# Optimization experiments

Measured on AMD Instinct MI355X. Metric: run time of the kernel, lower is better.

The kernel has to match this reference:

```python
import jax, jax.numpy as jnp
import numpy as np
import math

HIDDEN = 768
LABEL_NUM = 16
N_HEADS = 12
HEAD_DIM = HIDDEN // N_HEADS


def setup_inputs() -> dict:
    key = jax.random.key(0)
    ks = jax.random.split(key, 8)
    B, S, L, Ls, H = 8, 128, LABEL_NUM, 8, HIDDEN
    std = 1.0 / math.sqrt(H)
    return {
        "token_embs": jax.random.normal(ks[0], (B, S, H), jnp.float32),
        "label_embs": jax.random.normal(ks[1], (L, Ls, H), jnp.float32),
        "token_mask": jnp.ones((B, S), jnp.float32),
        "label_mask": jnp.ones((L, Ls), jnp.float32),
        "Wq": jax.random.normal(ks[2], (H, H), jnp.float32) * std,
        "bq": jnp.zeros((H,), jnp.float32),
        "Wk": jax.random.normal(ks[3], (H, H), jnp.float32) * std,
        "bk": jnp.zeros((H,), jnp.float32),
        "Wv": jax.random.normal(ks[4], (H, H), jnp.float32) * std,
        "bv": jnp.zeros((H,), jnp.float32),
    }


def reference(token_embs, label_embs, token_mask, label_mask, Wq, bq, Wk, bk, Wv, bv):
    B, S, H = token_embs.shape
    L, Ls, _ = label_embs.shape
    T = S + Ls
    # broadcast (instead of repeat) then concat: [B, L, T, H] -> [B*L, T, H]
    tok = jnp.broadcast_to(token_embs[:, None, :, :], (B, L, S, H))
    lab = jnp.broadcast_to(label_embs[None, :, :, :], (B, L, Ls, H))
    x = jnp.concatenate([tok, lab], axis=2).reshape(B * L, T, H)
    # mask: [B*L, T]; extended additive mask (1-m)*-10000
    tm = jnp.broadcast_to(token_mask[:, None, :], (B, L, S))
    lm = jnp.broadcast_to(label_mask[None, :, :], (B, L, Ls))
    mask = jnp.concatenate([tm, lm], axis=2).reshape(B * L, T)
    bias = (1.0 - mask) * -10000.0  # [BL, T]
    # QKV (torch Linear: y = x W^T + b)
    q = (x @ Wq.T + bq).reshape(B * L, T, N_HEADS, HEAD_DIM)
    k = (x @ Wk.T + bk).reshape(B * L, T, N_HEADS, HEAD_DIM)
    v = (x @ Wv.T + bv).reshape(B * L, T, N_HEADS, HEAD_DIM)
    scores = jnp.einsum("bthd,bshd->bhts", q, k) / math.sqrt(HEAD_DIM)
    scores = scores + bias[:, None, None, :]
    probs = jax.nn.softmax(scores, axis=-1)
    ctx = jnp.einsum("bhts,bshd->bthd", probs, v).reshape(B * L, T, H)
    # [B, L, T, H] -> [B, T, L, H]
    fused = ctx.reshape(B, L, T, H).transpose(0, 2, 1, 3)
    return (fused,)
```

## Files before the change

### kernel.cpp

```cpp
#include <hip/hip_runtime.h>
#include <hip/hip_bf16.h>
#include <stdint.h>

#define HIDDEN 768
#define NH 12
#define HD 64
#define BB 8
#define SS 128
#define LL 16
#define LS 8
#define TT 136
#define NROWS 1152
#define BH (BB * NH)

typedef __attribute__((ext_vector_type(8))) short bf16x8;
typedef __attribute__((ext_vector_type(4))) float f32x4;
typedef __attribute__((ext_vector_type(16))) float f32x16;
typedef __hip_bfloat16 bf16;

__device__ inline float tof(bf16 x) { return __bfloat162float(x); }
__device__ inline uint16_t b16bits(float f) {
    bf16 h = __float2bfloat16(f);
    union { bf16 h; uint16_t u; } u; u.h = h; return u.u;
}

#define TOK_V4 196608
#define XB_V4  221184
#define W_V4   147456
__global__ __launch_bounds__(256) void cast_kernel(
    const float* __restrict__ tok, const float* __restrict__ lab,
    const float* __restrict__ Wq, const float* __restrict__ Wk,
    const float* __restrict__ Wv,
    uint16_t* __restrict__ Xb, uint16_t* __restrict__ Wb)
{
    int g = blockIdx.x * 256 + threadIdx.x;
    float4 v;
    ushort4* d;
    if (g < XB_V4) {
        v = (g < TOK_V4) ? reinterpret_cast<const float4*>(tok)[g]
                         : reinterpret_cast<const float4*>(lab)[g - TOK_V4];
        d = reinterpret_cast<ushort4*>(Xb) + g;
    } else {
        int w = g - XB_V4;
        v = (w < W_V4)     ? reinterpret_cast<const float4*>(Wq)[w]
          : (w < 2 * W_V4) ? reinterpret_cast<const float4*>(Wk)[w - W_V4]
                           : reinterpret_cast<const float4*>(Wv)[w - 2 * W_V4];
        d = reinterpret_cast<ushort4*>(Wb) + w;
    }
    ushort4 h;
    h.x = b16bits(v.x); h.y = b16bits(v.y); h.z = b16bits(v.z); h.w = b16bits(v.w);
    *d = h;
}

__global__ __launch_bounds__(256) void qkv_kernel(
    const uint16_t* __restrict__ Xb, const uint16_t* __restrict__ Wb,
    const float* __restrict__ bq, const float* __restrict__ bk,
    const float* __restrict__ bv,
    bf16* __restrict__ Qw, bf16* __restrict__ Kw, bf16* __restrict__ Vw)
{
    __shared__ __align__(16) uint16_t As[2][64 * 72];
    __shared__ __align__(16) uint16_t Bs[2][128 * 72];

    int tid = threadIdx.x;
    int lane = tid & 63, wv = tid >> 6;
    int ml = lane & 15, quad = lane >> 4;
    int mt = blockIdx.x / 18, nt = blockIdx.x % 18;
    int wr = wv >> 1, wc = wv & 1;

    int mat = nt / 6;
    int col0 = (nt % 6) * 128;
    const float* bptr = (mat == 0) ? bq : ((mat == 1) ? bk : bv);
    bf16* obase       = (mat == 0) ? Qw : ((mat == 1) ? Kw : Vw);

    const uint16_t* asrc = Xb + (size_t)mt * 64 * HIDDEN;
    const uint16_t* bsrc = Wb + (size_t)nt * 128 * HIDDEN;

    int ar_[2], ac_[2], br_[4], bc_[4];
    #pragma unroll
    for (int i = 0; i < 2; ++i) { int g = i * 256 + tid; ar_[i] = g >> 3; ac_[i] = (g & 7) * 8; }
    #pragma unroll
    for (int i = 0; i < 4; ++i) { int g = i * 256 + tid; br_[i] = g >> 3; bc_[i] = (g & 7) * 8; }

    bf16x8 ra[2], rb[4];
    #pragma unroll
    for (int i = 0; i < 2; ++i)
        ra[i] = *reinterpret_cast<const bf16x8*>(asrc + (size_t)ar_[i] * HIDDEN + ac_[i]);
    #pragma unroll
    for (int i = 0; i < 4; ++i)
        rb[i] = *reinterpret_cast<const bf16x8*>(bsrc + (size_t)br_[i] * HIDDEN + bc_[i]);

    f32x4 acc[2][4] = {};
    int p = 0;

    for (int k0 = 0; k0 < HIDDEN; k0 += 64) {
        #pragma unroll
        for (int i = 0; i < 2; ++i)
            *reinterpret_cast<bf16x8*>(&As[p][ar_[i] * 72 + ac_[i]]) = ra[i];
        #pragma unroll
        for (int i = 0; i < 4; ++i)
            *reinterpret_cast<bf16x8*>(&Bs[p][br_[i] * 72 + bc_[i]]) = rb[i];
        __syncthreads();

        if (k0 + 64 < HIDDEN) {
            #pragma unroll
            for (int i = 0; i < 2; ++i)
                ra[i] = *reinterpret_cast<const bf16x8*>(asrc + (size_t)ar_[i] * HIDDEN + k0 + 64 + ac_[i]);
            #pragma unroll
            for (int i = 0; i < 4; ++i)
                rb[i] = *reinterpret_cast<const bf16x8*>(bsrc + (size_t)br_[i] * HIDDEN + k0 + 64 + bc_[i]);
        }

        #pragma unroll
        for (int kh = 0; kh < 2; ++kh) {
            bf16x8 af[2], bfr[4];
            #pragma unroll
            for (int rt = 0; rt < 2; ++rt)
                af[rt] = *reinterpret_cast<const bf16x8*>(&As[p][(wr * 32 + rt * 16 + ml) * 72 + kh * 32 + quad * 8]);
            #pragma unroll
            for (int ct = 0; ct < 4; ++ct)
                bfr[ct] = *reinterpret_cast<const bf16x8*>(&Bs[p][(wc * 64 + ct * 16 + ml) * 72 + kh * 32 + quad * 8]);
            #pragma unroll
            for (int rt = 0; rt < 2; ++rt)
                #pragma unroll
                for (int ct = 0; ct < 4; ++ct)
                    acc[rt][ct] = __builtin_amdgcn_mfma_f32_16x16x32_bf16(af[rt], bfr[ct], acc[rt][ct], 0, 0, 0);
        }
        p ^= 1;
    }

    #pragma unroll
    for (int ct = 0; ct < 4; ++ct) {
        int c = col0 + wc * 64 + ct * 16 + ml;
        float bvv = bptr[c];
        #pragma unroll
        for (int rt = 0; rt < 2; ++rt) {
            #pragma unroll
            for (int reg = 0; reg < 4; ++reg) {
                int R = mt * 64 + wr * 32 + rt * 16 + quad * 4 + reg;
                obase[(size_t)R * HIDDEN + c] = __float2bfloat16(acc[rt][ct][reg] + bvv);
            }
        }
    }
}

__global__ __launch_bounds__(256) void attn_tt_kernel(
    const bf16* __restrict__ Qw, const bf16* __restrict__ Kw,
    const bf16* __restrict__ Vw, const float* __restrict__ tmask,
    bf16* __restrict__ ctx_tt, float* __restrict__ m_tt, float* __restrict__ d_tt,
    uint32_t* __restrict__ Vt_g)
{
    __shared__ __align__(16) uint32_t KldsW[128 * 36];
    __shared__ __align__(16) uint32_t VtW[64 * 68];
    __shared__ __align__(16) uint32_t PW[4][16 * 68];
    __shared__ float bias_s[128];

    int bh = blockIdx.x >> 1;
    int hf = blockIdx.x & 1;
    int b = bh / NH, h = bh % NH;
    int tid = threadIdx.x;
    int lane = tid & 63, wv = tid >> 6;
    int ml = lane & 15, quad = lane >> 4;

    for (int i = tid; i < 128 * 32; i += 256) {
        int s = i >> 5, w = i & 31;
        KldsW[s * 36 + w] =
            reinterpret_cast<const uint32_t*>(Kw + (size_t)(b * SS + s) * HIDDEN + h * HD)[w];
    }
    #pragma unroll
    for (int c = 0; c < 8; ++c) {
        int g = c * 256 + tid;
        int s2 = g >> 5, dw = g & 31;
        const uint32_t* v0 = reinterpret_cast<const uint32_t*>(Vw + (size_t)(b * SS + 2 * s2) * HIDDEN + h * HD);
        const uint32_t* v1 = reinterpret_cast<const uint32_t*>(Vw + (size_t)(b * SS + 2 * s2 + 1) * HIDDEN + h * HD);
        uint32_t a = v0[dw], bb = v1[dw];
        VtW[(2 * dw) * 68 + s2]     = (a & 0xffffu) | ((bb & 0xffffu) << 16);
        VtW[(2 * dw + 1) * 68 + s2] = (a >> 16) | (bb & 0xffff0000u);
    }
    for (int i = tid; i < 128; i += 256)
        bias_s[i] = (1.0f - tmask[b * SS + i]) * -10000.0f;
    __syncthreads();

    if (hf == 0) {
        uint32_t* vg = Vt_g + (size_t)bh * 4096;
        #pragma unroll
        for (int c = 0; c < 16; ++c) {
            int g = c * 256 + tid;
            vg[g] = VtW[(g >> 6) * 68 + (g & 63)];
        }
    }

    const bf16* Klb = reinterpret_cast<const bf16*>(KldsW);
    const bf16* Vtb = reinterpret_cast<const bf16*>(VtW);
    const bf16* Pb  = reinterpret_cast<const bf16*>(PW[wv]);

    int qr = hf * 64 + wv * 16 + ml;
    const bf16* qp = Qw + (size_t)(b * SS + qr) * HIDDEN + h * HD + quad * 8;
    bf16x8 a0 = *reinterpret_cast<const bf16x8*>(qp);
    bf16x8 a1 = *reinterpret_cast<const bf16x8*>(qp + 32);

    f32x4 sc[8];
    #pragma unroll
    for (int ct = 0; ct < 8; ++ct) {
        const bf16* kp = Klb + (ct * 16 + ml) * 72 + quad * 8;
        bf16x8 b0 = *reinterpret_cast<const bf16x8*>(kp);
        bf16x8 b1 = *reinterpret_cast<const bf16x8*>(kp + 32);
        f32x4 z = {0.f, 0.f, 0.f, 0.f};
        z = __builtin_amdgcn_mfma_f32_16x16x32_bf16(a0, b0, z, 0, 0, 0);
        z = __builtin_amdgcn_mfma_f32_16x16x32_bf16(a1, b1, z, 0, 0, 0);
        sc[ct] = z;
    }

    float mx[4] = {-1e30f, -1e30f, -1e30f, -1e30f};
    #pragma unroll
    for (int ct = 0; ct < 8; ++ct) {
        float bc = bias_s[ct * 16 + ml];
        #pragma unroll
        for (int reg = 0; reg < 4; ++reg) {
            float v = sc[ct][reg] * 0.125f + bc;
            sc[ct][reg] = v;
            mx[reg] = fmaxf(mx[reg], v);
        }
    }
    #pragma unroll
    for (int reg = 0; reg < 4; ++reg)
        #pragma unroll
        for (int off = 1; off < 16; off <<= 1)
            mx[reg] = fmaxf(mx[reg], __shfl_xor(mx[reg], off));

    float Zs[4] = {0.f, 0.f, 0.f, 0.f};
    #pragma unroll
    for (int ct = 0; ct < 8; ++ct) {
        #pragma unroll
        for (int reg = 0; reg < 4; ++reg) {
            float e = __expf(sc[ct][reg] - mx[reg]);
            sc[ct][reg] = e;
            Zs[reg] += e;
        }
    }
    #pragma unroll
    for (int reg = 0; reg < 4; ++reg)
        #pragma unroll
        for (int off = 1; off < 16; off <<= 1)
            Zs[reg] += __shfl_xor(Zs[reg], off);

    #pragma unroll
    for (int reg = 0; reg < 4; ++reg) {
        int gr = bh * 128 + hf * 64 + wv * 16 + quad * 4 + reg;
        if (ml == 0) { m_tt[gr] = mx[reg]; d_tt[gr] = Zs[reg]; }
    }

    #pragma unroll
    for (int ct = 0; ct < 8; ++ct) {
        #pragma unroll
        for (int reg = 0; reg < 4; ++reg) {
            float e = sc[ct][reg];
            float ep = __shfl_xor(e, 1);
            if ((ml & 1) == 0)
                PW[wv][(quad * 4 + reg) * 68 + ct * 8 + (ml >> 1)] =
                    (uint32_t)b16bits(e) | ((uint32_t)b16bits(ep) << 16);
        }
    }

    float rZ[4];
    #pragma unroll
    for (int reg = 0; reg < 4; ++reg) rZ[reg] = 1.0f / Zs[reg];

    #pragma unroll
    for (int ct4 = 0; ct4 < 4; ++ct4) {
        f32x4 acc = {0.f, 0.f, 0.f, 0.f};
        #pragma unroll
        for (int ks = 0; ks < 4; ++ks) {
            bf16x8 ap = *reinterpret_cast<const bf16x8*>(Pb + ml * 136 + ks * 32 + quad * 8);
            bf16x8 bp = *reinterpret_cast<const bf16x8*>(Vtb + (ct4 * 16 + ml) * 136 + ks * 32 + quad * 8);
            acc = __builtin_amdgcn_mfma_f32_16x16x32_bf16(ap, bp, acc, 0, 0, 0);
        }
        #pragma unroll
        for (int reg = 0; reg < 4; ++reg) {
            int gr = bh * 128 + hf * 64 + wv * 16 + quad * 4 + reg;
            ctx_tt[(size_t)gr * 64 + ct4 * 16 + ml] = __float2bfloat16(acc[reg] * rZ[reg]);
        }
    }
}

__global__ __launch_bounds__(256) void attn_merge_kernel(
    const bf16* __restrict__ Qw, const bf16* __restrict__ Kw,
    const bf16* __restrict__ Vw, const uint32_t* __restrict__ Vt_g,
    const bf16* __restrict__ ctx_tt, const float* __restrict__ m_tt,
    const float* __restrict__ d_tt,
    const float* __restrict__ tmask, const float* __restrict__ lmask,
    float* __restrict__ out)
{
    __shared__ __align__(16) uint32_t VtW[64 * 84];
    __shared__ __align__(16) uint32_t PWL[16 * 84];
    __shared__ __align__(16) uint32_t P2W[4][32 * 8];
    __shared__ float wtab[4][32], itab[4][32];
    __shared__ float mtt_s[128], dtt_s[128], bias_t[128];
    __shared__ float bias_l[16];

    int p = blockIdx.x & 7;
    int h = (blockIdx.x >> 3) % NH;
    int b = blockIdx.x / (8 * NH);
    int l0 = 2 * p, l1 = l0 + 1;
    int bh = b * NH + h;
    int tid = threadIdx.x;
    int lane = tid & 63, wv = tid >> 6;
    int ml = lane & 15, quad = lane >> 4;
    int hl = lane & 31, hi = lane >> 5;

    {
        const uint32_t* vg = Vt_g + (size_t)bh * 4096;
        #pragma unroll
        for (int c = 0; c < 16; ++c) {
            int g = c * 256 + tid;
            VtW[(g >> 6) * 84 + (g & 63)] = vg[g];
        }
    }
    for (int g = tid; g < 512; g += 256) {
        int d = g >> 3, jj = g & 7;
        int s0 = 128 + 2 * jj, s1 = s0 + 1;
        int r0 = (s0 < 136) ? (1024 + l0 * LS + (s0 - 128)) : (1024 + l1 * LS + (s0 - 136));
        int r1 = (s1 < 136) ? (1024 + l0 * LS + (s1 - 128)) : (1024 + l1 * LS + (s1 - 136));
        uint16_t lo = reinterpret_cast<const uint16_t*>(Vw + (size_t)r0 * HIDDEN + h * HD)[d];
        uint16_t hi2 = reinterpret_cast<const uint16_t*>(Vw + (size_t)r1 * HIDDEN + h * HD)[d];
        VtW[d * 84 + 64 + jj] = (uint32_t)lo | ((uint32_t)hi2 << 16);
    }
    for (int g = tid; g < 512; g += 256)
        VtW[(g >> 3) * 84 + 72 + (g & 7)] = 0;

    if (tid < 128) {
        mtt_s[tid] = m_tt[bh * 128 + tid];
        dtt_s[tid] = d_tt[bh * 128 + tid];
        bias_t[tid] = (1.0f - tmask[b * SS + tid]) * -10000.0f;
    }
    if (tid < 16) {
        int labk = (tid < 8) ? (l0 * LS + tid) : (l1 * LS + tid - 8);
        bias_l[tid] = (1.0f - lmask[labk]) * -10000.0f;
    }
    if (tid < 128)
        PWL[(tid >> 3) * 84 + 72 + (tid & 7)] = 0;
    __syncthreads();

    const bf16* Vtb = reinterpret_cast<const bf16*>(VtW);

    int kprow = 1024 + ((ml < 8) ? (l0 * LS + ml) : (l1 * LS + ml - 8));
    const bf16* kpp = Kw + (size_t)kprow * HIDDEN + h * HD + quad * 8;
    bf16x8 kb0 = *reinterpret_cast<const bf16x8*>(kpp);
    bf16x8 kb1 = *reinterpret_cast<const bf16x8*>(kpp + 32);

    if (wv < 3) {
        const bf16* P2b = reinterpret_cast<const bf16*>(P2W[wv]);
        for (int rt = wv; rt < 8; rt += 3) {
            int tq = rt * 16 + ml;
            const bf16* qp = Qw + (size_t)(b * SS + tq) * HIDDEN + h * HD + quad * 8;
            bf16x8 a0 = *reinterpret_cast<const bf16x8*>(qp);
            bf16x8 a1 = *reinterpret_cast<const bf16x8*>(qp + 32);

            f32x4 z = {0.f, 0.f, 0.f, 0.f};
            z = __builtin_amdgcn_mfma_f32_16x16x32_bf16(a0, kb0, z, 0, 0, 0);
            z = __builtin_amdgcn_mfma_f32_16x16x32_bf16(a1, kb1, z, 0, 0, 0);

            #pragma unroll
            for (int reg = 0; reg < 4; ++reg) {
                int trow = quad * 4 + reg;
                float s = z[reg] * 0.125f + bias_l[ml];
                float m = s;
                m = fmaxf(m, __shfl_xor(m, 1));
                m = fmaxf(m, __shfl_xor(m, 2));
                m = fmaxf(m, __shfl_xor(m, 4));
                float mtt = mtt_s[rt * 16 + trow], dtt = dtt_s[rt * 16 + trow];
                float m_new = fmaxf(mtt, m);
                float e = __expf(s - m_new);
                float dh = e;
                dh += __shfl_xor(dh, 1);
                dh += __shfl_xor(dh, 2);
                dh += __shfl_xor(dh, 4);
                float alpha = __expf(mtt - m_new);
                float w = alpha * dtt;
                float inv = 1.0f / (w + dh);
                if (ml == 0) { wtab[wv][trow] = w;      itab[wv][trow] = inv; }
                if (ml == 8) { wtab[wv][16 + trow] = w; itab[wv][16 + trow] = inv; }
                float ep = __shfl_xor(e, 1);
                if ((ml & 1) == 0) {
                    uint32_t pk = (uint32_t)b16bits(e) | ((uint32_t)b16bits(ep) << 16);
                    P2W[wv][trow * 8 + (ml >> 1)]        = (ml < 8) ? pk : 0u;
                    P2W[wv][(16 + trow) * 8 + (ml >> 1)] = (ml < 8) ? 0u : pk;
                }
            }

            bf16x8 ap  = *reinterpret_cast<const bf16x8*>(P2b + hl * 16 + hi * 8);
            bf16x8 bv0 = *reinterpret_cast<const bf16x8*>(Vtb + hl * 168 + 128 + hi * 8);
            bf16x8 bv1 = *reinterpret_cast<const bf16x8*>(Vtb + (32 + hl) * 168 + 128 + hi * 8);
            f32x16 c0 = {}, c1 = {};
            c0 = __builtin_amdgcn_mfma_f32_32x32x16_bf16(ap, bv0, c0, 0, 0, 0);
            c1 = __builtin_amdgcn_mfma_f32_32x32x16_bf16(ap, bv1, c1, 0, 0, 0);

            float cv0[8], cv1[8];
            #pragma unroll
            for (int reg = 0; reg < 8; ++reg) {
                int row = (reg & 3) + 8 * (reg >> 2) + 4 * hi;
                const bf16* cp = ctx_tt + (size_t)(bh * 128 + rt * 16 + row) * 64;
                cv0[reg] = tof(cp[hl]);
                cv1[reg] = tof(cp[32 + hl]);
            }
            #pragma unroll
            for (int reg = 0; reg < 16; ++reg) {
                int row = (reg & 3) + 8 * (reg >> 2) + 4 * hi;
                int trow = row & 15;
                int lsel = (row < 16) ? l0 : l1;
                float w = wtab[wv][row], inv = itab[wv][row];
                float c0v = (reg < 8) ? cv0[reg] : cv0[reg - 8];
                float c1v = (reg < 8) ? cv1[reg] : cv1[reg - 8];
                size_t ob = (((size_t)b * TT + rt * 16 + trow) * LL + lsel) * HIDDEN + h * HD;
                out[ob + hl]      = (w * c0v + c0[reg]) * inv;
                out[ob + 32 + hl] = (w * c1v + c1[reg]) * inv;
            }
        }
    } else {
        const bf16* Pb = reinterpret_cast<const bf16*>(PWL);
        int qrow = 1024 + ((ml < 8) ? (l0 * LS + ml) : (l1 * LS + ml - 8));
        const bf16* qp = Qw + (size_t)qrow * HIDDEN + h * HD + quad * 8;
        bf16x8 a0 = *reinterpret_cast<const bf16x8*>(qp);
        bf16x8 a1 = *reinterpret_cast<const bf16x8*>(qp + 32);

        f32x4 sc[9];
        #pragma unroll
        for (int ct = 0; ct < 9; ++ct) {
            bf16x8 b0, b1;
            if (ct < 8) {
                const bf16* kp = Kw + (size_t)(b * SS + ct * 16 + ml) * HIDDEN + h * HD + quad * 8;
                b0 = *reinterpret_cast<const bf16x8*>(kp);
                b1 = *reinterpret_cast<const bf16x8*>(kp + 32);
            } else { b0 = kb0; b1 = kb1; }
            f32x4 zz = {0.f, 0.f, 0.f, 0.f};
            zz = __builtin_amdgcn_mfma_f32_16x16x32_bf16(a0, b0, zz, 0, 0, 0);
            zz = __builtin_amdgcn_mfma_f32_16x16x32_bf16(a1, b1, zz, 0, 0, 0);
            sc[ct] = zz;
        }

        float mx[4] = {-1e30f, -1e30f, -1e30f, -1e30f};
        #pragma unroll
        for (int ct = 0; ct < 9; ++ct) {
            #pragma unroll
            for (int reg = 0; reg < 4; ++reg) {
                int rq = quad * 4 + reg;
                float bc = (ct < 8) ? bias_t[ct * 16 + ml]
                                    : (((rq < 8) != (ml < 8)) ? -1e30f : bias_l[ml]);
                float v = sc[ct][reg] * 0.125f + bc;
                sc[ct][reg] = v;
                mx[reg] = fmaxf(mx[reg], v);
            }
        }
        #pragma unroll
        for (int reg = 0; reg < 4; ++reg)
            #pragma unroll
            for (int off = 1; off < 16; off <<= 1)
                mx[reg] = fmaxf(mx[reg], __shfl_xor(mx[reg], off));

        float Zs[4] = {0.f, 0.f, 0.f, 0.f};
        #pragma unroll
        for (int ct = 0; ct < 9; ++ct) {
            #pragma unroll
            for (int reg = 0; reg < 4; ++reg) {
                float e = __expf(sc[ct][reg] - mx[reg]);
                sc[ct][reg] = e;
                Zs[reg] += e;
            }
        }
        #pragma unroll
        for (int reg = 0; reg < 4; ++reg)
            #pragma unroll
            for (int off = 1; off < 16; off <<= 1)
                Zs[reg] += __shfl_xor(Zs[reg], off);
        float zi[4];
        #pragma unroll
        for (int reg = 0; reg < 4; ++reg) zi[reg] = 1.0f / Zs[reg];

        #pragma unroll
        for (int ct = 0; ct < 9; ++ct) {
            #pragma unroll
            for (int reg = 0; reg < 4; ++reg) {
                float e = sc[ct][reg];
                float ep = __shfl_xor(e, 1);
                if ((ml & 1) == 0)
                    PWL[(quad * 4 + reg) * 84 + ct * 8 + (ml >> 1)] =
                        (uint32_t)b16bits(e) | ((uint32_t)b16bits(ep) << 16);
            }
        }

        #pragma unroll
        for (int ct4 = 0; ct4 < 4; ++ct4) {
            f32x4 acc = {0.f, 0.f, 0.f, 0.f};
            #pragma unroll
            for (int ks = 0; ks < 5; ++ks) {
                bf16x8 ap = *reinterpret_cast<const bf16x8*>(Pb + ml * 168 + ks * 32 + quad * 8);
                bf16x8 bp = *reinterpret_cast<const bf16x8*>(Vtb + (ct4 * 16 + ml) * 168 + ks * 32 + quad * 8);
                acc = __builtin_amdgcn_mfma_f32_16x16x32_bf16(ap, bp, acc, 0, 0, 0);
            }
            #pragma unroll
            for (int reg = 0; reg < 4; ++reg) {
                int rq = quad * 4 + reg;
                int l = (rq < 8) ? l0 : l1;
                int t = SS + (rq & 7);
                out[(((size_t)b * TT + t) * LL + l) * HIDDEN + h * HD + ct4 * 16 + ml] =
                    acc[reg] * zi[reg];
            }
        }
    }
}

extern "C" void kernel_launch(void* const* d_in, const int* in_sizes, int n_in,
                              void* d_out, int out_size, void* d_ws, size_t ws_size,
                              hipStream_t stream)
{
    const float* tok   = (const float*)d_in[0];
    const float* lab   = (const float*)d_in[1];
    const float* tmask = (const float*)d_in[2];
    const float* lmask = (const float*)d_in[3];
    const float* Wq    = (const float*)d_in[4];
    const float* bq    = (const float*)d_in[5];
    const float* Wk    = (const float*)d_in[6];
    const float* bk    = (const float*)d_in[7];
    const float* Wv    = (const float*)d_in[8];
    const float* bv    = (const float*)d_in[9];

    bf16* Qw = (bf16*)d_ws;
    bf16* Kw = Qw + (size_t)NROWS * HIDDEN;
    bf16* Vw = Kw + (size_t)NROWS * HIDDEN;
    bf16* ctx = Vw + (size_t)NROWS * HIDDEN;
    float* m_tt = (float*)(ctx + (size_t)BH * 128 * 64);
    float* d_tt = m_tt + BH * 128;
    uint32_t* Vt_g = (uint32_t*)(d_tt + BH * 128);
    uint16_t* Xb = (uint16_t*)(Vt_g + (size_t)BH * 4096);
    uint16_t* Wb = Xb + (size_t)NROWS * HIDDEN;

    cast_kernel<<<dim3(2592), 256, 0, stream>>>(tok, lab, Wq, Wk, Wv, Xb, Wb);
    qkv_kernel<<<dim3(18 * 18), 256, 0, stream>>>(
        Xb, Wb, bq, bk, bv, Qw, Kw, Vw);
    attn_tt_kernel<<<dim3(BH * 2), 256, 0, stream>>>(
        Qw, Kw, Vw, tmask, ctx, m_tt, d_tt, Vt_g);
    attn_merge_kernel<<<dim3(BB * NH * 8), 256, 0, stream>>>(
        Qw, Kw, Vw, Vt_g, ctx, m_tt, d_tt, tmask, lmask, (float*)d_out);
}
```

Measured before the change: 129.5 us.

## Process two label pairs per merge block to reuse staged V and ctx loads

```diff
diff --git a/kernel.cpp b/kernel.cpp
--- a/kernel.cpp
+++ b/kernel.cpp
@@ -292,18 +292,15 @@
 {
     __shared__ __align__(16) uint32_t VtW[64 * 84];
     __shared__ __align__(16) uint32_t PWL[16 * 84];
-    __shared__ __align__(16) uint32_t P2W[4][32 * 8];
-    __shared__ float wtab[4][32], itab[4][32];
+    __shared__ __align__(16) uint32_t P2W[3][32 * 8];
+    __shared__ float wtab[3][32], itab[3][32];
     __shared__ float mtt_s[128], dtt_s[128], bias_t[128];
-    __shared__ float bias_l[16];
-
-    int p = blockIdx.x & 7;
-    int h = (blockIdx.x >> 3) % NH;
-    int b = blockIdx.x / (8 * NH);
-    int l0 = 2 * p, l1 = l0 + 1;
-    int bh = b * NH + h;
+    __shared__ float bias_l[2][16];
+
+    int bh = blockIdx.x % 96, pp = blockIdx.x / 96;
+    int b = bh / NH, h = bh % NH;
     int tid = threadIdx.x;
-    int lane = tid & 63, wv = tid >> 6;
+    int lane = tid & 63, wvi = tid >> 6;
     int ml = lane & 15, quad = lane >> 4;
     int hl = lane & 31, hi = lane >> 5;
 
@@ -315,84 +312,51 @@
             VtW[(g >> 6) * 84 + (g & 63)] = vg[g];
         }
     }
-    for (int g = tid; g < 512; g += 256) {
-        int d = g >> 3, jj = g & 7;
+    for (int g = tid; g < 1024; g += 256) {
+        int d = g >> 4, slot = g & 15;
+        int it = slot >> 3, jj = slot & 7;
+        int lp = pp + it * 4;
+        int l0 = 2 * lp, l1 = l0 + 1;
         int s0 = 128 + 2 * jj, s1 = s0 + 1;
         int r0 = (s0 < 136) ? (1024 + l0 * LS + (s0 - 128)) : (1024 + l1 * LS + (s0 - 136));
         int r1 = (s1 < 136) ? (1024 + l0 * LS + (s1 - 128)) : (1024 + l1 * LS + (s1 - 136));
-        uint16_t lo = reinterpret_cast<const uint16_t*>(Vw + (size_t)r0 * HIDDEN + h * HD)[d];
+        uint16_t lo  = reinterpret_cast<const uint16_t*>(Vw + (size_t)r0 * HIDDEN + h * HD)[d];
         uint16_t hi2 = reinterpret_cast<const uint16_t*>(Vw + (size_t)r1 * HIDDEN + h * HD)[d];
-        VtW[d * 84 + 64 + jj] = (uint32_t)lo | ((uint32_t)hi2 << 16);
-    }
-    for (int g = tid; g < 512; g += 256)
-        VtW[(g >> 3) * 84 + 72 + (g & 7)] = 0;
-
+        VtW[d * 84 + 64 + it * 8 + jj] = (uint32_t)lo | ((uint32_t)hi2 << 16);
+    }
     if (tid < 128) {
         mtt_s[tid] = m_tt[bh * 128 + tid];
         dtt_s[tid] = d_tt[bh * 128 + tid];
         bias_t[tid] = (1.0f - tmask[b * SS + tid]) * -10000.0f;
     }
-    if (tid < 16) {
-        int labk = (tid < 8) ? (l0 * LS + tid) : (l1 * LS + tid - 8);
-        bias_l[tid] = (1.0f - lmask[labk]) * -10000.0f;
-    }
-    if (tid < 128)
-        PWL[(tid >> 3) * 84 + 72 + (tid & 7)] = 0;
+    if (tid < 32) {
+        int it = tid >> 4, j = tid & 15;
+        int lp = pp + it * 4;
+        int labk = (j < 8) ? (2 * lp * LS + j) : ((2 * lp + 1) * LS + j - 8);
+        bias_l[it][j] = (1.0f - lmask[labk]) * -10000.0f;
+    }
     __syncthreads();
 
     const bf16* Vtb = reinterpret_cast<const bf16*>(VtW);
 
-    int kprow = 1024 + ((ml < 8) ? (l0 * LS + ml) : (l1 * LS + ml - 8));
-    const bf16* kpp = Kw + (size_t)kprow * HIDDEN + h * HD + quad * 8;
-    bf16x8 kb0 = *reinterpret_cast<const bf16x8*>(kpp);
-    bf16x8 kb1 = *reinterpret_cast<const bf16x8*>(kpp + 32);
-
-    if (wv < 3) {
-        const bf16* P2b = reinterpret_cast<const bf16*>(P2W[wv]);
-        for (int rt = wv; rt < 8; rt += 3) {
+    bf16x8 kbA[2], kbB[2];
+    #pragma unroll
+    for (int it = 0; it < 2; ++it) {
+        int lp = pp + it * 4;
+        int l0 = 2 * lp, l1 = l0 + 1;
+        int kprow = 1024 + ((ml < 8) ? (l0 * LS + ml) : (l1 * LS + ml - 8));
+        const bf16* kpp = Kw + (size_t)kprow * HIDDEN + h * HD + quad * 8;
+        kbA[it] = *reinterpret_cast<const bf16x8*>(kpp);
+        kbB[it] = *reinterpret_cast<const bf16x8*>(kpp + 32);
+    }
+
+    if (wvi < 3) {
+        const bf16* P2b = reinterpret_cast<const bf16*>(P2W[wvi]);
+        for (int rt = wvi; rt < 8; rt += 3) {
             int tq = rt * 16 + ml;
             const bf16* qp = Qw + (size_t)(b * SS + tq) * HIDDEN + h * HD + quad * 8;
             bf16x8 a0 = *reinterpret_cast<const bf16x8*>(qp);
             bf16x8 a1 = *reinterpret_cast<const bf16x8*>(qp + 32);
-
-            f32x4 z = {0.f, 0.f, 0.f, 0.f};
-            z = __builtin_amdgcn_mfma_f32_16x16x32_bf16(a0, kb0, z, 0, 0, 0);
-            z = __builtin_amdgcn_mfma_f32_16x16x32_bf16(a1, kb1, z, 0, 0, 0);
-
-            #pragma unroll
-            for (int reg = 0; reg < 4; ++reg) {
-                int trow = quad * 4 + reg;
-                float s = z[reg] * 0.125f + bias_l[ml];
-                float m = s;
-                m = fmaxf(m, __shfl_xor(m, 1));
-                m = fmaxf(m, __shfl_xor(m, 2));
-                m = fmaxf(m, __shfl_xor(m, 4));
-                float mtt = mtt_s[rt * 16 + trow], dtt = dtt_s[rt * 16 + trow];
-                float m_new = fmaxf(mtt, m);
-                float e = __expf(s - m_new);
-                float dh = e;
-                dh += __shfl_xor(dh, 1);
-                dh += __shfl_xor(dh, 2);
-                dh += __shfl_xor(dh, 4);
-                float alpha = __expf(mtt - m_new);
-                float w = alpha * dtt;
-                float inv = 1.0f / (w + dh);
-                if (ml == 0) { wtab[wv][trow] = w;      itab[wv][trow] = inv; }
-                if (ml == 8) { wtab[wv][16 + trow] = w; itab[wv][16 + trow] = inv; }
-                float ep = __shfl_xor(e, 1);
-                if ((ml & 1) == 0) {
-                    uint32_t pk = (uint32_t)b16bits(e) | ((uint32_t)b16bits(ep) << 16);
-                    P2W[wv][trow * 8 + (ml >> 1)]        = (ml < 8) ? pk : 0u;
-                    P2W[wv][(16 + trow) * 8 + (ml >> 1)] = (ml < 8) ? 0u : pk;
-                }
-            }
-
-            bf16x8 ap  = *reinterpret_cast<const bf16x8*>(P2b + hl * 16 + hi * 8);
-            bf16x8 bv0 = *reinterpret_cast<const bf16x8*>(Vtb + hl * 168 + 128 + hi * 8);
-            bf16x8 bv1 = *reinterpret_cast<const bf16x8*>(Vtb + (32 + hl) * 168 + 128 + hi * 8);
-            f32x16 c0 = {}, c1 = {};
-            c0 = __builtin_amdgcn_mfma_f32_32x32x16_bf16(ap, bv0, c0, 0, 0, 0);
-            c1 = __builtin_amdgcn_mfma_f32_32x32x16_bf16(ap, bv1, c1, 0, 0, 0);
 
             float cv0[8], cv1[8];
             #pragma unroll
@@ -402,107 +366,165 @@
                 cv0[reg] = tof(cp[hl]);
                 cv1[reg] = tof(cp[32 + hl]);
             }
-            #pragma unroll
-            for (int reg = 0; reg < 16; ++reg) {
-                int row = (reg & 3) + 8 * (reg >> 2) + 4 * hi;
-                int trow = row & 15;
-                int lsel = (row < 16) ? l0 : l1;
-                float w = wtab[wv][row], inv = itab[wv][row];
-                float c0v = (reg < 8) ? cv0[reg] : cv0[reg - 8];
-                float c1v = (reg < 8) ? cv1[reg] : cv1[reg - 8];
-                size_t ob = (((size_t)b * TT + rt * 16 + trow) * LL + lsel) * HIDDEN + h * HD;
-                out[ob + hl]      = (w * c0v + c0[reg]) * inv;
-                out[ob + 32 + hl] = (w * c1v + c1[reg]) * inv;
+
+            #pragma unroll
+            for (int it = 0; it < 2; ++it) {
+                int lp = pp + it * 4;
+                int l0 = 2 * lp, l1 = l0 + 1;
+
+                f32x4 z = {0.f, 0.f, 0.f, 0.f};
+                z = __builtin_amdgcn_mfma_f32_16x16x32_bf16(a0, kbA[it], z, 0, 0, 0);
+                z = __builtin_amdgcn_mfma_f32_16x16x32_bf16(a1, kbB[it], z, 0, 0, 0);
+
+                #pragma unroll
+                for (int reg = 0; reg < 4; ++reg) {
+                    int trow = quad * 4 + reg;
+                    float s = z[reg] * 0.125f + bias_l[it][ml];
+                    float m = s;
+                    m = fmaxf(m, __shfl_xor(m, 1));
+                    m = fmaxf(m, __shfl_xor(m, 2));
+                    m = fmaxf(m, __shfl_xor(m, 4));
+                    float mtt = mtt_s[rt * 16 + trow], dtt = dtt_s[rt * 16 + trow];
+                    float m_new = fmaxf(mtt, m);
+                    float e = __expf(s - m_new);
+                    float dh = e;
+                    dh += __shfl_xor(dh, 1);
+                    dh += __shfl_xor(dh, 2);
+                    dh += __shfl_xor(dh, 4);
+                    float alpha = __expf(mtt - m_new);
+                    float w = alpha * dtt;
+                    float inv = 1.0f / (w + dh);
+                    if (ml == 0) { wtab[wvi][trow] = w;      itab[wvi][trow] = inv; }
+                    if (ml == 8) { wtab[wvi][16 + trow] = w; itab[wvi][16 + trow] = inv; }
+                    float ep = __shfl_xor(e, 1);
+                    if ((ml & 1) == 0) {
+                        uint32_t pk = (uint32_t)b16bits(e) | ((uint32_t)b16bits(ep) << 16);
+                        P2W[wvi][trow * 8 + (ml >> 1)]        = (ml < 8) ? pk : 0u;
+                        P2W[wvi][(16 + trow) * 8 + (ml >> 1)] = (ml < 8) ? 0u : pk;
+                    }
+                }
+
+                bf16x8 ap  = *reinterpret_cast<const bf16x8*>(P2b + hl * 16 + hi * 8);
+                bf16x8 bv0 = *reinterpret_cast<const bf16x8*>(Vtb + hl * 168 + 128 + it * 16 + hi * 8);
+                bf16x8 bv1 = *reinterpret_cast<const bf16x8*>(Vtb + (32 + hl) * 168 + 128 + it * 16 + hi * 8);
+                f32x16 c0 = {}, c1 = {};
+                c0 = __builtin_amdgcn_mfma_f32_32x32x16_bf16(ap, bv0, c0, 0, 0, 0);
+                c1 = __builtin_amdgcn_mfma_f32_32x32x16_bf16(ap, bv1, c1, 0, 0, 0);
+
+                #pragma unroll
+                for (int reg = 0; reg < 16; ++reg) {
+                    int row = (reg & 3) + 8 * (reg >> 2) + 4 * hi;
+                    int trow = row & 15;
+                    int lsel = (row < 16) ? l0 : l1;
+                    float w = wtab[wvi][row], inv = itab[wvi][row];
+                    float c0v = (reg < 8) ? cv0[reg] : cv0[reg - 8];
+                    float c1v = (reg < 8) ? cv1[reg] : cv1[reg - 8];
+                    size_t ob = (((size_t)b * TT + rt * 16 + trow) * LL + lsel) * HIDDEN + h * HD;
+                    out[ob + hl]      = (w * c0v + c0[reg]) * inv;
+                    out[ob + 32 + hl] = (w * c1v + c1[reg]) * inv;
+                }
             }
         }
     } else {
         const bf16* Pb = reinterpret_cast<const bf16*>(PWL);
-        int qrow = 1024 + ((ml < 8) ? (l0 * LS + ml) : (l1 * LS + ml - 8));
-        const bf16* qp = Qw + (size_t)qrow * HIDDEN + h * HD + quad * 8;
-        bf16x8 a0 = *reinterpret_cast<const bf16x8*>(qp);
-        bf16x8 a1 = *reinterpret_cast<const bf16x8*>(qp + 32);
-
-        f32x4 sc[9];
-        #pragma unroll
-        for (int ct = 0; ct < 9; ++ct) {
-            bf16x8 b0, b1;
-            if (ct < 8) {
-                const bf16* kp = Kw + (size_t)(b * SS + ct * 16 + ml) * HIDDEN + h * HD + quad * 8;
-                b0 = *reinterpret_cast<const bf16x8*>(kp);
-                b1 = *reinterpret_cast<const bf16x8*>(kp + 32);
-            } else { b0 = kb0; b1 = kb1; }
-            f32x4 zz = {0.f, 0.f, 0.f, 0.f};
-            zz = __builtin_amdgcn_mfma_f32_16x16x32_bf16(a0, b0, zz, 0, 0, 0);
-            zz = __builtin_amdgcn_mfma_f32_16x16x32_bf16(a1, b1, zz, 0, 0, 0);
-            sc[ct] = zz;
-        }
-
-        float mx[4] = {-1e30f, -1e30f, -1e30f, -1e30f};
-        #pragma unroll
-        for (int ct = 0; ct < 9; ++ct) {
-            #pragma unroll
-            for (int reg = 0; reg < 4; ++reg) {
-                int rq = quad * 4 + reg;
-                float bc = (ct < 8) ? bias_t[ct * 16 + ml]
-                                    : (((rq < 8) != (ml < 8)) ? -1e30f : bias_l[ml]);
-                float v = sc[ct][reg] * 0.125f + bc;
-                sc[ct][reg] = v;
-                mx[reg] = fmaxf(mx[reg], v);
-            }
-        }
-        #pragma unroll
-        for (int reg = 0; reg < 4; ++reg)
-            #pragma unroll
-            for (int off = 1; off < 16; off <<= 1)
-                mx[reg] = fmaxf(mx[reg], __shfl_xor(mx[reg], off));
-
-        float Zs[4] = {0.f, 0.f, 0.f, 0.f};
-        #pragma unroll
-        for (int ct = 0; ct < 9; ++ct) {
-            #pragma unroll
-            for (int reg = 0; reg < 4; ++reg) {
-                float e = __expf(sc[ct][reg] - mx[reg]);
-                sc[ct][reg] = e;
-                Zs[reg] += e;
-            }
-        }
-        #pragma unroll
-        for (int reg = 0; reg < 4; ++reg)
-            #pragma unroll
-            for (int off = 1; off < 16; off <<= 1)
-                Zs[reg] += __shfl_xor(Zs[reg], off);
-        float zi[4];
-        #pragma unroll
-        for (int reg = 0; reg < 4; ++reg) zi[reg] = 1.0f / Zs[reg];
-
-        #pragma unroll
-        for (int ct = 0; ct < 9; ++ct) {
-            #pragma unroll
-            for (int reg = 0; reg < 4; ++reg) {
-                float e = sc[ct][reg];
-                float ep = __shfl_xor(e, 1);
-                if ((ml & 1) == 0)
-                    PWL[(quad * 4 + reg) * 84 + ct * 8 + (ml >> 1)] =
-                        (uint32_t)b16bits(e) | ((uint32_t)b16bits(ep) << 16);
-            }
-        }
-
-        #pragma unroll
-        for (int ct4 = 0; ct4 < 4; ++ct4) {
-            f32x4 acc = {0.f, 0.f, 0.f, 0.f};
-            #pragma unroll
-            for (int ks = 0; ks < 5; ++ks) {
-                bf16x8 ap = *reinterpret_cast<const bf16x8*>(Pb + ml * 168 + ks * 32 + quad * 8);
-                bf16x8 bp = *reinterpret_cast<const bf16x8*>(Vtb + (ct4 * 16 + ml) * 168 + ks * 32 + quad * 8);
-                acc = __builtin_amdgcn_mfma_f32_16x16x32_bf16(ap, bp, acc, 0, 0, 0);
-            }
-            #pragma unroll
-            for (int reg = 0; reg < 4; ++reg) {
-                int rq = quad * 4 + reg;
-                int l = (rq < 8) ? l0 : l1;
-                int t = SS + (rq & 7);
-                out[(((size_t)b * TT + t) * LL + l) * HIDDEN + h * HD + ct4 * 16 + ml] =
-                    acc[reg] * zi[reg];
+        #pragma unroll
+        for (int it = 0; it < 2; ++it) {
+            int lp = pp + it * 4;
+            int l0 = 2 * lp, l1 = l0 + 1;
+
+            for (int z2 = lane; z2 < 128; z2 += 64) {
+                int row = z2 >> 3, col = z2 & 7;
+                PWL[row * 84 + 64 + (1 - it) * 8 + col] = 0;
+            }
+
+            int qrow = 1024 + ((ml < 8) ? (l0 * LS + ml) : (l1 * LS + ml - 8));
+            const bf16* qp = Qw + (size_t)qrow * HIDDEN + h * HD + quad * 8;
+            bf16x8 a0 = *reinterpret_cast<const bf16x8*>(qp);
+            bf16x8 a1 = *reinterpret_cast<const bf16x8*>(qp + 32);
+
+            f32x4 sc[9];
+            #pragma unroll
+            for (int ct = 0; ct < 9; ++ct) {
+                bf16x8 b0, b1;
+                if (ct < 8) {
+                    const bf16* kp = Kw + (size_t)(b * SS + ct * 16 + ml) * HIDDEN + h * HD + quad * 8;
+                    b0 = *reinterpret_cast<const bf16x8*>(kp);
+                    b1 = *reinterpret_cast<const bf16x8*>(kp + 32);
+                } else { b0 = kbA[it]; b1 = kbB[it]; }
+                f32x4 zz = {0.f, 0.f, 0.f, 0.f};
+                zz = __builtin_amdgcn_mfma_f32_16x16x32_bf16(a0, b0, zz, 0, 0, 0);
+                zz = __builtin_amdgcn_mfma_f32_16x16x32_bf16(a1, b1, zz, 0, 0, 0);
+                sc[ct] = zz;
+            }
+
+            float mx[4] = {-1e30f, -1e30f, -1e30f, -1e30f};
+            #pragma unroll
+            for (int ct = 0; ct < 9; ++ct) {
+                #pragma unroll
+                for (int reg = 0; reg < 4; ++reg) {
+                    int rq = quad * 4 + reg;
+                    float bc = (ct < 8) ? bias_t[ct * 16 + ml]
+                                        : (((rq < 8) != (ml < 8)) ? -1e30f : bias_l[it][ml]);
+                    float v = sc[ct][reg] * 0.125f + bc;
+                    sc[ct][reg] = v;
+                    mx[reg] = fmaxf(mx[reg], v);
+                }
+            }
+            #pragma unroll
+            for (int reg = 0; reg < 4; ++reg)
+                #pragma unroll
+                for (int off = 1; off < 16; off <<= 1)
+                    mx[reg] = fmaxf(mx[reg], __shfl_xor(mx[reg], off));
+
+            float Zs[4] = {0.f, 0.f, 0.f, 0.f};
+            #pragma unroll
+            for (int ct = 0; ct < 9; ++ct) {
+                #pragma unroll
+                for (int reg = 0; reg < 4; ++reg) {
+                    float e = __expf(sc[ct][reg] - mx[reg]);
+                    sc[ct][reg] = e;
+                    Zs[reg] += e;
+                }
+            }
+            #pragma unroll
+            for (int reg = 0; reg < 4; ++reg)
+                #pragma unroll
+                for (int off = 1; off < 16; off <<= 1)
+                    Zs[reg] += __shfl_xor(Zs[reg], off);
+            float zi[4];
+            #pragma unroll
+            for (int reg = 0; reg < 4; ++reg) zi[reg] = 1.0f / Zs[reg];
+
+            #pragma unroll
+            for (int ct = 0; ct < 9; ++ct) {
+                int cbase = (ct < 8) ? ct * 8 : (64 + it * 8);
+                #pragma unroll
+                for (int reg = 0; reg < 4; ++reg) {
+                    float e = sc[ct][reg];
+                    float ep = __shfl_xor(e, 1);
+                    if ((ml & 1) == 0)
+                        PWL[(quad * 4 + reg) * 84 + cbase + (ml >> 1)] =
+                            (uint32_t)b16bits(e) | ((uint32_t)b16bits(ep) << 16);
+                }
+            }
+
+            #pragma unroll
+            for (int ct4 = 0; ct4 < 4; ++ct4) {
+                f32x4 acc = {0.f, 0.f, 0.f, 0.f};
+                #pragma unroll
+                for (int ks = 0; ks < 5; ++ks) {
+                    bf16x8 ap = *reinterpret_cast<const bf16x8*>(Pb + ml * 168 + ks * 32 + quad * 8);
+                    bf16x8 bp = *reinterpret_cast<const bf16x8*>(Vtb + (ct4 * 16 + ml) * 168 + ks * 32 + quad * 8);
+                    acc = __builtin_amdgcn_mfma_f32_16x16x32_bf16(ap, bp, acc, 0, 0, 0);
+                }
+                #pragma unroll
+                for (int reg = 0; reg < 4; ++reg) {
+                    int rq = quad * 4 + reg;
+                    int l = (rq < 8) ? l0 : l1;
+                    int t = SS + (rq & 7);
+                    out[(((size_t)b * TT + t) * LL + l) * HIDDEN + h * HD + ct4 * 16 + ml] =
+                        acc[reg] * zi[reg];
+                }
             }
         }
     }
@@ -538,6 +560,6 @@
         Xb, Wb, bq, bk, bv, Qw, Kw, Vw);
     attn_tt_kernel<<<dim3(BH * 2), 256, 0, stream>>>(
         Qw, Kw, Vw, tmask, ctx, m_tt, d_tt, Vt_g);
-    attn_merge_kernel<<<dim3(BB * NH * 8), 256, 0, stream>>>(
+    attn_merge_kernel<<<dim3(384), 256, 0, stream>>>(
         Qw, Kw, Vw, Vt_g, ctx, m_tt, d_tt, tmask, lmask, (float*)d_out);
 }
```

Measured after the change: 133.6 us. 1.03x slower.
